# Optimization experiments

Hardware: AMD Instinct MI355X
Metric: run time of the kernel (lower is better)

## Reference

```python
import jax, jax.numpy as jnp
import numpy as np

DELTA = 0.5  # EMA coefficient from __init__
B, N, CAT, FEAT, K = 8, 32768, 128, 128, 64


def setup_inputs() -> dict:
    key = jax.random.key(0)
    k1, k2 = jax.random.split(key)
    inp = jax.random.normal(k1, (B, N, CAT), dtype=jnp.float32)
    # nn.init.constant(weight, 1/sqrt(in_features))
    weight = jnp.full((CAT, FEAT), 1.0 / np.sqrt(FEAT), dtype=jnp.float32)
    keys = jnp.arange(K, dtype=jnp.int32)  # unique feat_dict keys, in [0, category)
    values = jax.random.normal(k2, (K, FEAT), dtype=jnp.float32)
    return {"input": inp, "weight": weight, "keys": keys, "values": values}


def reference(input, weight, keys, values):
    # output = (input @ weight).permute(0, 2, 1): (B, N, CAT) x (CAT, FEAT) -> (B, FEAT, N)
    output = jnp.einsum('bnc,cf->bfn', input, weight)
    # Per-key EMA update followed by scalar-L2-norm row overwrite (faithful to
    # torch: weight[key] = ||delta*w_k + (1-delta)*v_k||_2 broadcast over the row).
    new_rows = DELTA * weight[keys] + (1.0 - DELTA) * values           # (K, FEAT)
    norms = jnp.sqrt(jnp.sum(new_rows * new_rows, axis=1, keepdims=True))  # (K, 1)
    new_weight = weight.at[keys].set(jnp.broadcast_to(norms, new_rows.shape))
    return output, new_weight
```

## Files before the change

kernel.cpp:

```cpp
#include <hip/hip_runtime.h>
#include <math.h>

constexpr int B_ = 8, N_ = 32768, CAT_ = 128, FEAT_ = 128, K_ = 64;
constexpr float DELTA_ = 0.5f;

typedef __bf16 bf16x8 __attribute__((ext_vector_type(8)));
typedef float f32x4 __attribute__((ext_vector_type(4)));

constexpr int LDSTR = 136;
constexpr int GEMM_BLOCKS = (B_ * N_) / 128;

__global__ __launch_bounds__(256, 4) void ocm_fused(
    const float* __restrict__ input,
    const float* __restrict__ weight,
    const int* __restrict__ keys,
    const float* __restrict__ values,
    float* __restrict__ out)
{
    const int bid = blockIdx.x;
    const int tid = threadIdx.x;

    if (bid >= GEMM_BLOCKS) {
        float* outw = out + (size_t)B_ * FEAT_ * N_;
        const int r = bid - GEMM_BLOCKS;
        bool keyed = false;
        for (int i = 0; i < K_; ++i) keyed |= (keys[i] == r);
        if (!keyed && tid < FEAT_)
            outw[r * FEAT_ + tid] = weight[r * FEAT_ + tid];
        if (r < K_ && tid < 64) {
            const int key = keys[r];
            float a0 = DELTA_ * weight[key * FEAT_ + tid]      + (1.0f - DELTA_) * values[r * FEAT_ + tid];
            float a1 = DELTA_ * weight[key * FEAT_ + tid + 64] + (1.0f - DELTA_) * values[r * FEAT_ + tid + 64];
            float ss = a0 * a0 + a1 * a1;
            #pragma unroll
            for (int off = 32; off > 0; off >>= 1)
                ss += __shfl_down(ss, off, 64);
            float nrm = sqrtf(__shfl(ss, 0, 64));
            outw[key * FEAT_ + tid]      = nrm;
            outw[key * FEAT_ + tid + 64] = nrm;
        }
        return;
    }

    __shared__ __bf16 wt[FEAT_ * LDSTR];

    #pragma unroll
    for (int j = 0; j < (CAT_ * FEAT_) / 256; ++j) {
        int i = tid + j * 256;
        int c = i >> 7;
        int f = i & (FEAT_ - 1);
        wt[f * LDSTR + c] = (__bf16)weight[i];
    }
    __syncthreads();

    const int wid  = tid >> 6;
    const int lane = tid & 63;
    const int qlo  = lane & 15;
    const int qhi  = lane >> 4;
    const int b    = bid >> 8;
    const int nb   = bid & 255;
    const int n0   = nb * 128 + wid * 32;

    f32x4 acc[8][2];
    #pragma unroll
    for (int i = 0; i < 8; ++i)
        #pragma unroll
        for (int j = 0; j < 2; ++j)
            acc[i][j] = (f32x4)0.0f;

    const float* in_base = input + ((size_t)b * N_ + n0) * CAT_;

    #pragma unroll
    for (int ck = 0; ck < 4; ++ck) {
        bf16x8 bfrag[2];
        #pragma unroll
        for (int nt = 0; nt < 2; ++nt) {
            const float* p = in_base + (size_t)(nt * 16 + qlo) * CAT_ + ck * 32 + qhi * 8;
            f32x4 v0 = *(const f32x4*)p;
            f32x4 v1 = *(const f32x4*)(p + 4);
            bf16x8 t;
            t[0] = (__bf16)v0[0]; t[1] = (__bf16)v0[1]; t[2] = (__bf16)v0[2]; t[3] = (__bf16)v0[3];
            t[4] = (__bf16)v1[0]; t[5] = (__bf16)v1[1]; t[6] = (__bf16)v1[2]; t[7] = (__bf16)v1[3];
            bfrag[nt] = t;
        }
        #pragma unroll
        for (int mt = 0; mt < 8; ++mt) {
            bf16x8 afrag = *(const bf16x8*)&wt[(mt * 16 + qlo) * LDSTR + ck * 32 + qhi * 8];
            acc[mt][0] = __builtin_amdgcn_mfma_f32_16x16x32_bf16(afrag, bfrag[0], acc[mt][0], 0, 0, 0);
            acc[mt][1] = __builtin_amdgcn_mfma_f32_16x16x32_bf16(afrag, bfrag[1], acc[mt][1], 0, 0, 0);
        }
    }

    float* outp = out + (size_t)b * FEAT_ * N_ + n0;
    #pragma unroll
    for (int mt = 0; mt < 8; ++mt) {
        #pragma unroll
        for (int nt = 0; nt < 2; ++nt) {
            #pragma unroll
            for (int r = 0; r < 4; ++r) {
                int f = mt * 16 + qhi * 4 + r;
                outp[(size_t)f * N_ + nt * 16 + qlo] = acc[mt][nt][r];
            }
        }
    }
}

extern "C" void kernel_launch(void* const* d_in, const int* in_sizes, int n_in,
                              void* d_out, int out_size, void* d_ws, size_t ws_size,
                              hipStream_t stream) {
    const float* input  = (const float*)d_in[0];
    const float* weight = (const float*)d_in[1];
    const int*   keys   = (const int*)d_in[2];
    const float* values = (const float*)d_in[3];
    float* out = (float*)d_out;
    ocm_fused<<<GEMM_BLOCKS + CAT_, 256, 0, stream>>>(input, weight, keys, values, out);
}
```

Before: 55.23 us.

## Split weight transpose into prep kernel and read bf16 weight from global in GEMM

```diff
diff --git a/kernel.cpp b/kernel.cpp
--- a/kernel.cpp
+++ b/kernel.cpp
@@ -7,8 +7,102 @@
 typedef __bf16 bf16x8 __attribute__((ext_vector_type(8)));
 typedef float f32x4 __attribute__((ext_vector_type(4)));
 
+constexpr int GEMM_BLOCKS = (B_ * N_) / 128;
+
+__global__ void prep_kernel(const float* __restrict__ weight,
+                            const int* __restrict__ keys,
+                            const float* __restrict__ values,
+                            float* __restrict__ outw,
+                            __bf16* __restrict__ wT)
+{
+    const int r = blockIdx.x;
+    const int t = threadIdx.x;
+    float w = weight[r * FEAT_ + t];
+    wT[t * CAT_ + r] = (__bf16)w;
+
+    bool keyed = false;
+    for (int i = 0; i < K_; ++i) keyed |= (keys[i] == r);
+    if (!keyed) outw[r * FEAT_ + t] = w;
+
+    if (r < K_ && t < 64) {
+        const int key = keys[r];
+        float a0 = DELTA_ * weight[key * FEAT_ + t]      + (1.0f - DELTA_) * values[r * FEAT_ + t];
+        float a1 = DELTA_ * weight[key * FEAT_ + t + 64] + (1.0f - DELTA_) * values[r * FEAT_ + t + 64];
+        float ss = a0 * a0 + a1 * a1;
+        #pragma unroll
+        for (int off = 32; off > 0; off >>= 1)
+            ss += __shfl_down(ss, off, 64);
+        float nrm = sqrtf(__shfl(ss, 0, 64));
+        outw[key * FEAT_ + t]      = nrm;
+        outw[key * FEAT_ + t + 64] = nrm;
+    }
+}
+
+__global__ __launch_bounds__(256, 4) void gemm_kernel(
+    const float* __restrict__ input,
+    const __bf16* __restrict__ wT,
+    float* __restrict__ out)
+{
+    const int bid  = blockIdx.x;
+    const int tid  = threadIdx.x;
+    const int wid  = tid >> 6;
+    const int lane = tid & 63;
+    const int qlo  = lane & 15;
+    const int qhi  = lane >> 4;
+    const int b    = bid >> 8;
+    const int nb   = bid & 255;
+    const int n0   = nb * 128 + wid * 32;
+
+    f32x4 acc[8][2];
+    #pragma unroll
+    for (int i = 0; i < 8; ++i)
+        #pragma unroll
+        for (int j = 0; j < 2; ++j)
+            acc[i][j] = (f32x4)0.0f;
+
+    const float* in_base = input + ((size_t)b * N_ + n0) * CAT_;
+
+    #pragma unroll
+    for (int ck = 0; ck < 4; ++ck) {
+        bf16x8 af[8];
+        #pragma unroll
+        for (int mt = 0; mt < 8; ++mt)
+            af[mt] = *(const bf16x8*)&wT[(mt * 16 + qlo) * CAT_ + ck * 32 + qhi * 8];
+
+        bf16x8 bfrag[2];
+        #pragma unroll
+        for (int nt = 0; nt < 2; ++nt) {
+            const float* p = in_base + (size_t)(nt * 16 + qlo) * CAT_ + ck * 32 + qhi * 8;
+            f32x4 v0 = *(const f32x4*)p;
+            f32x4 v1 = *(const f32x4*)(p + 4);
+            bf16x8 t;
+            t[0] = (__bf16)v0[0]; t[1] = (__bf16)v0[1]; t[2] = (__bf16)v0[2]; t[3] = (__bf16)v0[3];
+            t[4] = (__bf16)v1[0]; t[5] = (__bf16)v1[1]; t[6] = (__bf16)v1[2]; t[7] = (__bf16)v1[3];
+            bfrag[nt] = t;
+        }
+
+        #pragma unroll
+        for (int mt = 0; mt < 8; ++mt) {
+            acc[mt][0] = __builtin_amdgcn_mfma_f32_16x16x32_bf16(af[mt], bfrag[0], acc[mt][0], 0, 0, 0);
+            acc[mt][1] = __builtin_amdgcn_mfma_f32_16x16x32_bf16(af[mt], bfrag[1], acc[mt][1], 0, 0, 0);
+        }
+    }
+
+    float* outp = out + (size_t)b * FEAT_ * N_ + n0;
+    #pragma unroll
+    for (int mt = 0; mt < 8; ++mt) {
+        #pragma unroll
+        for (int nt = 0; nt < 2; ++nt) {
+            #pragma unroll
+            for (int r = 0; r < 4; ++r) {
+                int f = mt * 16 + qhi * 4 + r;
+                outp[(size_t)f * N_ + nt * 16 + qlo] = acc[mt][nt][r];
+            }
+        }
+    }
+}
+
 constexpr int LDSTR = 136;
-constexpr int GEMM_BLOCKS = (B_ * N_) / 128;
 
 __global__ __launch_bounds__(256, 4) void ocm_fused(
     const float* __restrict__ input,
@@ -43,7 +137,6 @@
     }
 
     __shared__ __bf16 wt[FEAT_ * LDSTR];
-
     #pragma unroll
     for (int j = 0; j < (CAT_ * FEAT_) / 256; ++j) {
         int i = tid + j * 256;
@@ -113,5 +206,13 @@
     const int*   keys   = (const int*)d_in[2];
     const float* values = (const float*)d_in[3];
     float* out = (float*)d_out;
-    ocm_fused<<<GEMM_BLOCKS + CAT_, 256, 0, stream>>>(input, weight, keys, values, out);
-}
+
+    if (ws_size >= (size_t)CAT_ * FEAT_ * sizeof(__bf16)) {
+        __bf16* wT = (__bf16*)d_ws;
+        float* outw = out + (size_t)B_ * FEAT_ * N_;
+        prep_kernel<<<CAT_, FEAT_, 0, stream>>>(weight, keys, values, outw, wT);
+        gemm_kernel<<<GEMM_BLOCKS, 256, 0, stream>>>(input, wT, out);
+    } else {
+        ocm_fused<<<GEMM_BLOCKS + CAT_, 256, 0, stream>>>(input, weight, keys, values, out);
+    }
+}
```

Result: slower. 91.54 us (+65.7%).
